# Optimization experiments

Measured on AMD Instinct MI355X. Metric: run time of the kernel, lower is better.

The kernel has to match this reference:

```python
import jax, jax.numpy as jnp
import numpy as np

HEADS = 8

def setup_inputs() -> dict:
    key = jax.random.key(0)
    ks = jax.random.split(key, 6)
    d = 256
    x = jax.random.normal(ks[0], (1, 8, 96, 96, d), dtype=jnp.float32)
    w_qkv = jax.random.normal(ks[1], (3 * d, d), dtype=jnp.float32) * (d ** -0.5)
    w_out = jax.random.normal(ks[2], (d, d), dtype=jnp.float32) * (d ** -0.5)
    b_out = jax.random.normal(ks[3], (d,), dtype=jnp.float32) * 0.01
    w_lin = jax.random.normal(ks[4], (d, d), dtype=jnp.float32) * (d ** -0.5)
    b_lin = jax.random.normal(ks[5], (d,), dtype=jnp.float32) * 0.01
    return {"x": x, "w_qkv": w_qkv, "w_out": w_out, "b_out": b_out,
            "w_lin": w_lin, "b_lin": b_lin}


def reference(x, w_qkv, w_out, b_out, w_lin, b_lin):
    b, t, h, w, d = x.shape
    dh = d // HEADS
    scale = dh ** -0.5
    n = h * w
    # fold time into batch; per-frame spatial tokens: [bf, n, d]
    xf = x.reshape(b * t, n, d)
    # 1x1 conv to_qkv (no bias) == matmul
    qkv = jnp.einsum('bnd,ed->bne', xf, w_qkv)          # [bf, n, 3d]
    q, k, v = jnp.split(qkv, 3, axis=-1)
    def to_heads(z):  # 'b (h c) xy' head-major split -> [bf, H, dh, n]
        return z.reshape(b * t, n, HEADS, dh).transpose(0, 2, 3, 1)
    q, k, v = map(to_heads, (q, k, v))
    q = jax.nn.softmax(q, axis=-2) * scale              # softmax over channel dim
    k = jax.nn.softmax(k, axis=-1)                      # softmax over spatial dim
    ctx = jnp.einsum('bhdn,bhen->bhde', k, v)           # [bf, H, dh, dh]
    out = jnp.einsum('bhde,bhdn->bhen', ctx, q)         # [bf, H, dh, n]
    out = out.transpose(0, 3, 1, 2).reshape(b * t, n, HEADS * dh)  # head-major merge
    out = out @ w_out.T + b_out                          # to_out 1x1 conv
    out = out.reshape(b, t, h, w, d)
    out = out @ w_lin.T + b_lin                          # fresh nn.Linear(d, d)
    return out + x                                       # residual skip
```

## Files before the change

kernel.cpp:

```cpp
#include <hip/hip_runtime.h>

using u16 = unsigned short;
typedef __attribute__((ext_vector_type(8))) short short8;
typedef __attribute__((ext_vector_type(4))) float f32x4;

__device__ __forceinline__ float b2f(u16 u){ union{unsigned u; float f;} c; c.u = ((unsigned)u) << 16; return c.f; }
__device__ __forceinline__ u16 f2b(float f){
  union{float f; unsigned u;} c; c.f = f;
  unsigned r = 0x7fffu + ((c.u >> 16) & 1u);
  return (u16)((c.u + r) >> 16);
}

#define GLOAD_LDS16(g, l) __builtin_amdgcn_global_load_lds( \
  (const __attribute__((address_space(1))) unsigned int*)(g), \
  (__attribute__((address_space(3))) unsigned int*)(l), 16, 0, 0)

__global__ void k_cvt(const float4* __restrict__ in, ushort4* __restrict__ out, int n4){
  int i = blockIdx.x * 256 + threadIdx.x;
  if (i < n4){
    float4 v = in[i];
    ushort4 o; o.x = f2b(v.x); o.y = f2b(v.y); o.z = f2b(v.z); o.w = f2b(v.w);
    out[i] = o;
  }
}

__global__ __launch_bounds__(256) void k_cvtw(const float* __restrict__ w, u16* __restrict__ out){
  int r = blockIdx.x, c = threadIdx.x;
  int src;
  if (r < 256) src = r;
  else { int g = r - 256, p4 = g >> 7, o = g & 127;
         src = (o < 64) ? 256 + p4*64 + o : 512 + p4*64 + (o - 64); }
  out[r*256 + c] = f2b(w[src*256 + c]);
}

__global__ __launch_bounds__(256) void k_prepw(const float* __restrict__ w_lin, const float* __restrict__ w_out,
    const float* __restrict__ b_out, const float* __restrict__ b_lin,
    float* __restrict__ wcf, float* __restrict__ bc){
  int l = blockIdx.x, i = threadIdx.x;
  float s = 0.f;
  for (int j = 0; j < 256; ++j) s += w_lin[l*256 + j] * w_out[j*256 + i];
  wcf[l*256 + i] = s;
  __shared__ float red[256];
  red[i] = w_lin[l*256 + i] * b_out[i];
  __syncthreads();
  for (int off = 128; off > 0; off >>= 1){ if (i < off) red[i] += red[i + off]; __syncthreads(); }
  if (i == 0) bc[l] = red[0] + b_lin[l];
}

__global__ __launch_bounds__(256, 3) void k_gemm_qkv(const u16* __restrict__ A, const u16* __restrict__ B,
    u16* __restrict__ qs, float* __restrict__ ctxu, float* __restrict__ zu, int M){
  constexpr int K = 256, NT = 8;
  __shared__ __align__(16) u16 pool[24576];
  u16* As = pool;
  u16* Bs = pool + 12288;
  const int t = threadIdx.x;
  const int wave = t >> 6, lane = t & 63;
  const int bi = blockIdx.x;
  const int xk = bi & 7, bj = bi >> 3;
  const int bm = (xk + 8*(bj/6)) * 128;
  const int bn = bj % 6;
  const int srow = wave*32 + (lane>>2);
  const int skel = (((lane&3) ^ ((lane>>3)&3)) << 3);
  const u16* ag = A + (size_t)(bm + srow)*K + skel;
  const u16* bg = B + (size_t)(bn*128 + srow)*K + skel;
  const size_t rstep = (size_t)16*K;
  const int wr = (wave>>1)*64, wc4 = (wave&1)*64;
  const int fr = lane & 15;
  const int fkc = lane >> 4;
  const int koff = ((fkc ^ ((fr>>1)&3)) << 3);
  f32x4 acc[4][4] = {};
  #pragma unroll
  for (int pre = 0; pre < 2; ++pre){
    u16* asl = As + pre*4096 + wave*1024; u16* bsl = Bs + pre*4096 + wave*1024;
    const int k0 = pre*32;
    GLOAD_LDS16(ag + k0,         asl);
    GLOAD_LDS16(ag + rstep + k0, asl + 512);
    GLOAD_LDS16(bg + k0,         bsl);
    GLOAD_LDS16(bg + rstep + k0, bsl + 512);
  }
  #pragma unroll
  for (int it = 0; it < NT; ++it){
    const int cur = it % 3;
    if (it == NT-1) { asm volatile("s_waitcnt vmcnt(0)" ::: "memory"); }
    else            { asm volatile("s_waitcnt vmcnt(4)" ::: "memory"); }
    __builtin_amdgcn_s_barrier();
    __builtin_amdgcn_sched_barrier(0);
    short8 av[4], bv[4];
    #pragma unroll
    for (int m = 0; m < 4; ++m)
      av[m] = *(const short8*)&As[cur*4096 + (wr + m*16 + fr)*32 + koff];
    #pragma unroll
    for (int n = 0; n < 4; ++n)
      bv[n] = *(const short8*)&Bs[cur*4096 + (wc4 + n*16 + fr)*32 + koff];
    if (it + 2 < NT){
      const int nb = (it+2) % 3;
      u16* asl = As + nb*4096 + wave*1024; u16* bsl = Bs + nb*4096 + wave*1024;
      const int k0 = (it+2)*32;
      GLOAD_LDS16(ag + k0,         asl);
      GLOAD_LDS16(ag + rstep + k0, asl + 512);
      GLOAD_LDS16(bg + k0,         bsl);
      GLOAD_LDS16(bg + rstep + k0, bsl + 512);
    }
    __builtin_amdgcn_s_setprio(1);
    #pragma unroll
    for (int m = 0; m < 4; ++m)
      #pragma unroll
      for (int n = 0; n < 4; ++n)
        acc[m][n] = __builtin_amdgcn_mfma_f32_16x16x32_bf16(av[m], bv[n], acc[m][n], 0, 0, 0);
    __builtin_amdgcn_s_setprio(0);
  }
  __syncthreads();
  const int lr0 = wr + (lane>>4)*4;
  if (bn < 2){
    u16* cmat = pool;
    #pragma unroll
    for (int m = 0; m < 4; ++m)
      #pragma unroll
      for (int n = 0; n < 4; ++n)
        #pragma unroll
        for (int r = 0; r < 4; ++r)
          cmat[(lr0 + m*16 + r)*136 + wc4 + n*16 + fr] = f2b(acc[m][n][r]);
    __syncthreads();
    const int row = t >> 1, co = (t & 1) * 64;
    #pragma unroll
    for (int hh = 0; hh < 2; ++hh){
      float f[32];
      #pragma unroll
      for (int c4 = 0; c4 < 4; ++c4){
        short8 w = *(const short8*)&cmat[row*136 + co + hh*32 + c4*8];
        #pragma unroll
        for (int k2 = 0; k2 < 8; ++k2) f[c4*8+k2] = b2f((u16)w[k2]);
      }
      float sum = 0.f;
      #pragma unroll
      for (int i2 = 0; i2 < 32; ++i2){ float e = __expf(f[i2]); f[i2] = e; sum += e; }
      float sc = 0.17677669529663689f / sum;
      #pragma unroll
      for (int c4 = 0; c4 < 4; ++c4){
        short8 o;
        #pragma unroll
        for (int k2 = 0; k2 < 8; ++k2) o[k2] = (short)f2b(f[c4*8+k2] * sc);
        *(short8*)&qs[(size_t)(bm+row)*256 + bn*128 + co + hh*32 + c4*8] = o;
      }
    }
  } else {
    u16* ekT = pool;
    u16* vT  = pool + 64*136;
    const bool isK = (wc4 == 0);
    #pragma unroll
    for (int m = 0; m < 4; ++m)
      #pragma unroll
      for (int n = 0; n < 4; ++n)
        #pragma unroll
        for (int r = 0; r < 4; ++r){
          int row = lr0 + m*16 + r;
          int csub = n*16 + fr;
          if (isK) ekT[csub*136 + row] = f2b(__expf(acc[m][n][r]));
          else     vT [csub*136 + row] = f2b(acc[m][n][r]);
        }
    __syncthreads();
    const int hl = wave >> 1, ti = wave & 1;
    const int head = (bn - 2)*2 + hl;
    short8 ones;
    #pragma unroll
    for (int j = 0; j < 8; ++j) ones[j] = (short)0x3F80;
    f32x4 acc2[2] = {}; f32x4 zacc = {};
    #pragma unroll
    for (int kc = 0; kc < 4; ++kc){
      const int ko2 = kc*32 + fkc*8;
      short8 av2 = *(const short8*)&ekT[(hl*32 + ti*16 + fr)*136 + ko2];
      short8 bv0 = *(const short8*)&vT [(hl*32 +         fr)*136 + ko2];
      short8 bv1 = *(const short8*)&vT [(hl*32 + 16 +    fr)*136 + ko2];
      acc2[0] = __builtin_amdgcn_mfma_f32_16x16x32_bf16(av2, bv0, acc2[0], 0, 0, 0);
      acc2[1] = __builtin_amdgcn_mfma_f32_16x16x32_bf16(av2, bv1, acc2[1], 0, 0, 0);
      zacc    = __builtin_amdgcn_mfma_f32_16x16x32_bf16(av2, ones, zacc, 0, 0, 0);
    }
    const int frame = bm / 9216;
    float* cb = ctxu + ((size_t)frame*8 + head)*1024;
    const int drow = ti*16 + (lane>>4)*4;
    #pragma unroll
    for (int tj = 0; tj < 2; ++tj)
      #pragma unroll
      for (int rr = 0; rr < 4; ++rr)
        atomicAdd(&cb[(drow + rr)*32 + tj*16 + fr], acc2[tj][rr]);
    if (fr == 0){
      float* zb = zu + ((size_t)frame*8 + head)*32;
      #pragma unroll
      for (int rr = 0; rr < 4; ++rr)
        atomicAdd(&zb[drow + rr], zacc[rr]);
    }
  }
}

__global__ __launch_bounds__(256, 3) void k_gemm_out(const u16* __restrict__ A, const u16* __restrict__ B,
    float* __restrict__ Cf, const float* __restrict__ bias, const u16* __restrict__ residb,
    int M, int NB, int frame_rows){
  constexpr int K = 256, N = 256, NT = 8;
  __shared__ __align__(16) u16 pool[24576];
  u16* As = pool;
  u16* Bs = pool + 12288;
  const int t = threadIdx.x;
  const int wave = t >> 6, lane = t & 63;
  const int bi = blockIdx.x;
  const int xk = bi & 7, bj = bi >> 3;
  const int bm = (xk + 8*(bj/NB)) * 128, bn = (bj%NB) * 128;
  if (frame_rows > 0) B += (size_t)(bm / frame_rows) * N * K;
  const int srow = wave*32 + (lane>>2);
  const int skel = (((lane&3) ^ ((lane>>3)&3)) << 3);
  const u16* ag = A + (size_t)(bm + srow)*K + skel;
  const u16* bg = B + (size_t)(bn + srow)*K + skel;
  const size_t rstep = (size_t)16*K;
  const int wr = (wave>>1)*64, wc4 = (wave&1)*64;
  const int fr = lane & 15;
  const int fkc = lane >> 4;
  const int koff = ((fkc ^ ((fr>>1)&3)) << 3);
  f32x4 acc[4][4] = {};
  #pragma unroll
  for (int pre = 0; pre < 2; ++pre){
    u16* asl = As + pre*4096 + wave*1024; u16* bsl = Bs + pre*4096 + wave*1024;
    const int k0 = pre*32;
    GLOAD_LDS16(ag + k0,         asl);
    GLOAD_LDS16(ag + rstep + k0, asl + 512);
    GLOAD_LDS16(bg + k0,         bsl);
    GLOAD_LDS16(bg + rstep + k0, bsl + 512);
  }
  #pragma unroll
  for (int it = 0; it < NT; ++it){
    const int cur = it % 3;
    if (it == NT-1) { asm volatile("s_waitcnt vmcnt(0)" ::: "memory"); }
    else            { asm volatile("s_waitcnt vmcnt(4)" ::: "memory"); }
    __builtin_amdgcn_s_barrier();
    __builtin_amdgcn_sched_barrier(0);
    short8 av[4], bv[4];
    #pragma unroll
    for (int m = 0; m < 4; ++m)
      av[m] = *(const short8*)&As[cur*4096 + (wr + m*16 + fr)*32 + koff];
    #pragma unroll
    for (int n = 0; n < 4; ++n)
      bv[n] = *(const short8*)&Bs[cur*4096 + (wc4 + n*16 + fr)*32 + koff];
    if (it + 2 < NT){
      const int nb = (it+2) % 3;
      u16* asl = As + nb*4096 + wave*1024; u16* bsl = Bs + nb*4096 + wave*1024;
      const int k0 = (it+2)*32;
      GLOAD_LDS16(ag + k0,         asl);
      GLOAD_LDS16(ag + rstep + k0, asl + 512);
      GLOAD_LDS16(bg + k0,         bsl);
      GLOAD_LDS16(bg + rstep + k0, bsl + 512);
    }
    __builtin_amdgcn_s_setprio(1);
    #pragma unroll
    for (int m = 0; m < 4; ++m)
      #pragma unroll
      for (int n = 0; n < 4; ++n)
        acc[m][n] = __builtin_amdgcn_mfma_f32_16x16x32_bf16(av[m], bv[n], acc[m][n], 0, 0, 0);
    __builtin_amdgcn_s_setprio(0);
  }
  __syncthreads();
  float* cmatf = (float*)pool;
  const int lr0 = (lane>>4)*4;
  float biasr[32];
  {
    const int c0 = bn + (t&3)*32;
    #pragma unroll
    for (int c4 = 0; c4 < 8; ++c4)
      *(float4*)&biasr[c4*4] = *(const float4*)&bias[c0 + c4*4];
  }
  #pragma unroll
  for (int half = 0; half < 2; ++half){
    if ((wr >> 6) == half){
      #pragma unroll
      for (int m = 0; m < 4; ++m)
        #pragma unroll
        for (int n = 0; n < 4; ++n)
          #pragma unroll
          for (int r = 0; r < 4; ++r)
            cmatf[(lr0 + m*16 + r)*132 + wc4 + n*16 + fr] = acc[m][n][r];
    }
    __syncthreads();
    {
      const int row = t >> 2, seg = (t & 3) * 32;
      const int gr = bm + half*64 + row;
      const size_t gbase = (size_t)gr*256 + bn + seg;
      float v[32];
      #pragma unroll
      for (int c4 = 0; c4 < 8; ++c4)
        *(float4*)&v[c4*4] = *(const float4*)&cmatf[row*132 + seg + c4*4];
      #pragma unroll
      for (int c4 = 0; c4 < 4; ++c4){
        short8 rr = *(const short8*)&residb[gbase + c4*8];
        #pragma unroll
        for (int k2 = 0; k2 < 8; ++k2)
          v[c4*8+k2] += biasr[c4*8+k2] + b2f((u16)rr[k2]);
      }
      #pragma unroll
      for (int c4 = 0; c4 < 8; ++c4)
        *(float4*)&Cf[gbase + c4*4] = *(float4*)&v[c4*4];
    }
    __syncthreads();
  }
}

__global__ __launch_bounds__(256) void k_weff(const float* __restrict__ ctxu, const float* __restrict__ zu,
    const float* __restrict__ wcf, u16* __restrict__ weff){
  int l = blockIdx.x, frel = blockIdx.y, t = threadIdx.x;
  int h = t >> 5, dd = t & 31;
  const float* cr = ctxu + (size_t)frel*8192 + h*1024 + dd*32;
  const float* wr = wcf + (size_t)l*256 + h*32;
  float s = 0.f;
  #pragma unroll
  for (int e = 0; e < 32; ++e) s += cr[e] * wr[e];
  float iz = 1.0f / zu[frel*256 + t];
  weff[((size_t)frel*256 + l)*256 + t] = f2b(s * iz);
}

extern "C" void kernel_launch(void* const* d_in, const int* in_sizes, int n_in,
                              void* d_out, int out_size, void* d_ws, size_t ws_size,
                              hipStream_t stream){
  const float* x     = (const float*)d_in[0];
  const float* w_qkv = (const float*)d_in[1];
  const float* w_out = (const float*)d_in[2];
  const float* b_out = (const float*)d_in[3];
  const float* w_lin = (const float*)d_in[4];
  const float* b_lin = (const float*)d_in[5];
  float* out = (float*)d_out;

  char* p = (char*)d_ws;
  u16*   wqb   = (u16*)p;   p += (size_t)768*256*2;
  float* wcf   = (float*)p; p += (size_t)256*256*4;
  float* bc    = (float*)p; p += 256*4;
  float* ctxu  = (float*)p; p += (size_t)8*8192*4;
  float* zu    = (float*)p; p += (size_t)8*256*4;
  u16*   weffb = (u16*)p;   p += (size_t)8*256*256*2;
  size_t fixed = (size_t)(p - (char*)d_ws);
  size_t per_frame = (size_t)2 * 9216*256*2;
  int chunk = (ws_size >= fixed + 8*per_frame) ? 8 : 1;
  u16* xb  = (u16*)p;
  u16* qsb = xb  + (size_t)chunk*9216*256;

  hipMemsetAsync(ctxu, 0, (size_t)8*8192*4 + (size_t)8*256*4, stream);

  hipLaunchKernelGGL(k_cvtw, dim3(768), dim3(256), 0, stream, w_qkv, wqb);
  hipLaunchKernelGGL(k_prepw, dim3(256), dim3(256), 0, stream, w_lin, w_out, b_out, b_lin, wcf, bc);

  for (int f0 = 0; f0 < 8; f0 += chunk){
    const float* xc = x  + (size_t)f0*9216*256;
    float*       oc = out + (size_t)f0*9216*256;
    const int M = chunk * 9216;
    const int n4 = M * 256 / 4;
    hipLaunchKernelGGL(k_cvt, dim3((n4 + 255)/256), dim3(256), 0, stream, (const float4*)xc, (ushort4*)xb, n4);
    hipLaunchKernelGGL(k_gemm_qkv, dim3((M/128)*6), dim3(256), 0, stream,
                       xb, wqb, qsb, ctxu + (size_t)f0*8192, zu + (size_t)f0*256, M);
    hipLaunchKernelGGL(k_weff, dim3(256, chunk), dim3(256), 0, stream,
                       ctxu + (size_t)f0*8192, zu + (size_t)f0*256, wcf, weffb + (size_t)f0*256*256);
    hipLaunchKernelGGL(k_gemm_out, dim3((M/128)*2), dim3(256), 0, stream,
                       qsb, weffb + (size_t)f0*256*256, oc, bc, xb,
                       M, 2, (chunk == 8) ? 9216 : 0);
  }
}
```

Before: 146.6 us.

## Spread ctx atomics over 8 slots, pack LDS stores, merge prep kernels

Atomic accumulation of the per-frame context and normaliser now goes to one of 8 replicated slots chosen by row tile, which reduces contention on each address. k_weff sums the slots before the projection. The K/V transpose stores into LDS are packed as 4 bf16 values in a uint2 instead of scalar u16 writes. The two weight-prep kernels are merged into one launch. The cost is a larger memset and slot reduction reads in k_weff.

```diff
diff --git a/kernel.cpp b/kernel.cpp
--- a/kernel.cpp
+++ b/kernel.cpp
@@ -24,27 +24,28 @@
   }
 }
 
-__global__ __launch_bounds__(256) void k_cvtw(const float* __restrict__ w, u16* __restrict__ out){
-  int r = blockIdx.x, c = threadIdx.x;
-  int src;
-  if (r < 256) src = r;
-  else { int g = r - 256, p4 = g >> 7, o = g & 127;
-         src = (o < 64) ? 256 + p4*64 + o : 512 + p4*64 + (o - 64); }
-  out[r*256 + c] = f2b(w[src*256 + c]);
-}
-
-__global__ __launch_bounds__(256) void k_prepw(const float* __restrict__ w_lin, const float* __restrict__ w_out,
+__global__ __launch_bounds__(256) void k_prep(const float* __restrict__ w,
+    const float* __restrict__ w_lin, const float* __restrict__ w_out,
     const float* __restrict__ b_out, const float* __restrict__ b_lin,
-    float* __restrict__ wcf, float* __restrict__ bc){
-  int l = blockIdx.x, i = threadIdx.x;
-  float s = 0.f;
-  for (int j = 0; j < 256; ++j) s += w_lin[l*256 + j] * w_out[j*256 + i];
-  wcf[l*256 + i] = s;
-  __shared__ float red[256];
-  red[i] = w_lin[l*256 + i] * b_out[i];
-  __syncthreads();
-  for (int off = 128; off > 0; off >>= 1){ if (i < off) red[i] += red[i + off]; __syncthreads(); }
-  if (i == 0) bc[l] = red[0] + b_lin[l];
+    u16* __restrict__ wq, float* __restrict__ wcf, float* __restrict__ bc){
+  int r = blockIdx.x, i = threadIdx.x;
+  if (r < 768){
+    int src;
+    if (r < 256) src = r;
+    else { int g = r - 256, p4 = g >> 7, o = g & 127;
+           src = (o < 64) ? 256 + p4*64 + o : 512 + p4*64 + (o - 64); }
+    wq[r*256 + i] = f2b(w[src*256 + i]);
+  } else {
+    int l = r - 768;
+    float s = 0.f;
+    for (int j = 0; j < 256; ++j) s += w_lin[l*256 + j] * w_out[j*256 + i];
+    wcf[l*256 + i] = s;
+    __shared__ float red[256];
+    red[i] = w_lin[l*256 + i] * b_out[i];
+    __syncthreads();
+    for (int off = 128; off > 0; off >>= 1){ if (i < off) red[i] += red[i + off]; __syncthreads(); }
+    if (i == 0) bc[l] = red[0] + b_lin[l];
+  }
 }
 
 __global__ __launch_bounds__(256, 3) void k_gemm_qkv(const u16* __restrict__ A, const u16* __restrict__ B,
@@ -147,17 +148,23 @@
     u16* ekT = pool;
     u16* vT  = pool + 64*136;
     const bool isK = (wc4 == 0);
-    #pragma unroll
-    for (int m = 0; m < 4; ++m)
-      #pragma unroll
-      for (int n = 0; n < 4; ++n)
-        #pragma unroll
-        for (int r = 0; r < 4; ++r){
-          int row = lr0 + m*16 + r;
-          int csub = n*16 + fr;
-          if (isK) ekT[csub*136 + row] = f2b(__expf(acc[m][n][r]));
-          else     vT [csub*136 + row] = f2b(acc[m][n][r]);
+    u16* dst = isK ? ekT : vT;
+    #pragma unroll
+    for (int m = 0; m < 4; ++m)
+      #pragma unroll
+      for (int n = 0; n < 4; ++n){
+        const int row = lr0 + m*16;
+        const int csub = n*16 + fr;
+        uint2 pk;
+        if (isK){
+          pk.x = (unsigned)f2b(__expf(acc[m][n][0])) | ((unsigned)f2b(__expf(acc[m][n][1])) << 16);
+          pk.y = (unsigned)f2b(__expf(acc[m][n][2])) | ((unsigned)f2b(__expf(acc[m][n][3])) << 16);
+        } else {
+          pk.x = (unsigned)f2b(acc[m][n][0]) | ((unsigned)f2b(acc[m][n][1]) << 16);
+          pk.y = (unsigned)f2b(acc[m][n][2]) | ((unsigned)f2b(acc[m][n][3]) << 16);
         }
+        *(uint2*)&dst[csub*136 + row] = pk;
+      }
     __syncthreads();
     const int hl = wave >> 1, ti = wave & 1;
     const int head = (bn - 2)*2 + hl;
@@ -176,7 +183,8 @@
       zacc    = __builtin_amdgcn_mfma_f32_16x16x32_bf16(av2, ones, zacc, 0, 0, 0);
     }
     const int frame = bm / 9216;
-    float* cb = ctxu + ((size_t)frame*8 + head)*1024;
+    const int slot = ((bm % 9216) >> 7) & 7;
+    float* cb = ctxu + (((size_t)frame*8 + slot)*8 + head)*1024;
     const int drow = ti*16 + (lane>>4)*4;
     #pragma unroll
     for (int tj = 0; tj < 2; ++tj)
@@ -184,7 +192,7 @@
       for (int rr = 0; rr < 4; ++rr)
         atomicAdd(&cb[(drow + rr)*32 + tj*16 + fr], acc2[tj][rr]);
     if (fr == 0){
-      float* zb = zu + ((size_t)frame*8 + head)*32;
+      float* zb = zu + (((size_t)frame*8 + slot)*8 + head)*32;
       #pragma unroll
       for (int rr = 0; rr < 4; ++rr)
         atomicAdd(&zb[drow + rr], zacc[rr]);
@@ -304,13 +312,23 @@
     const float* __restrict__ wcf, u16* __restrict__ weff){
   int l = blockIdx.x, frel = blockIdx.y, t = threadIdx.x;
   int h = t >> 5, dd = t & 31;
-  const float* cr = ctxu + (size_t)frel*8192 + h*1024 + dd*32;
+  float c[32];
+  #pragma unroll
+  for (int e = 0; e < 32; ++e) c[e] = 0.f;
+  #pragma unroll
+  for (int sl = 0; sl < 8; ++sl){
+    const float* cr = ctxu + (((size_t)frel*8 + sl)*8 + h)*1024 + dd*32;
+    #pragma unroll
+    for (int e = 0; e < 32; ++e) c[e] += cr[e];
+  }
+  float z = 0.f;
+  #pragma unroll
+  for (int sl = 0; sl < 8; ++sl) z += zu[(((size_t)frel*8 + sl)*8 + h)*32 + dd];
   const float* wr = wcf + (size_t)l*256 + h*32;
   float s = 0.f;
   #pragma unroll
-  for (int e = 0; e < 32; ++e) s += cr[e] * wr[e];
-  float iz = 1.0f / zu[frel*256 + t];
-  weff[((size_t)frel*256 + l)*256 + t] = f2b(s * iz);
+  for (int e = 0; e < 32; ++e) s += c[e] * wr[e];
+  weff[((size_t)frel*256 + l)*256 + t] = f2b(s / z);
 }
 
 extern "C" void kernel_launch(void* const* d_in, const int* in_sizes, int n_in,
@@ -328,8 +346,8 @@
   u16*   wqb   = (u16*)p;   p += (size_t)768*256*2;
   float* wcf   = (float*)p; p += (size_t)256*256*4;
   float* bc    = (float*)p; p += 256*4;
-  float* ctxu  = (float*)p; p += (size_t)8*8192*4;
-  float* zu    = (float*)p; p += (size_t)8*256*4;
+  float* ctxu  = (float*)p; p += (size_t)8*8*8192*4;
+  float* zu    = (float*)p; p += (size_t)8*8*256*4;
   u16*   weffb = (u16*)p;   p += (size_t)8*256*256*2;
   size_t fixed = (size_t)(p - (char*)d_ws);
   size_t per_frame = (size_t)2 * 9216*256*2;
@@ -337,10 +355,10 @@
   u16* xb  = (u16*)p;
   u16* qsb = xb  + (size_t)chunk*9216*256;
 
-  hipMemsetAsync(ctxu, 0, (size_t)8*8192*4 + (size_t)8*256*4, stream);
-
-  hipLaunchKernelGGL(k_cvtw, dim3(768), dim3(256), 0, stream, w_qkv, wqb);
-  hipLaunchKernelGGL(k_prepw, dim3(256), dim3(256), 0, stream, w_lin, w_out, b_out, b_lin, wcf, bc);
+  hipMemsetAsync(ctxu, 0, (size_t)8*8*8192*4 + (size_t)8*8*256*4, stream);
+
+  hipLaunchKernelGGL(k_prep, dim3(1024), dim3(256), 0, stream,
+                     w_qkv, w_lin, w_out, b_out, b_lin, wqb, wcf, bc);
 
   for (int f0 = 0; f0 < 8; f0 += chunk){
     const float* xc = x  + (size_t)f0*9216*256;
@@ -349,9 +367,9 @@
     const int n4 = M * 256 / 4;
     hipLaunchKernelGGL(k_cvt, dim3((n4 + 255)/256), dim3(256), 0, stream, (const float4*)xc, (ushort4*)xb, n4);
     hipLaunchKernelGGL(k_gemm_qkv, dim3((M/128)*6), dim3(256), 0, stream,
-                       xb, wqb, qsb, ctxu + (size_t)f0*8192, zu + (size_t)f0*256, M);
+                       xb, wqb, qsb, ctxu + (size_t)f0*8*8192, zu + (size_t)f0*8*256, M);
     hipLaunchKernelGGL(k_weff, dim3(256, chunk), dim3(256), 0, stream,
-                       ctxu + (size_t)f0*8192, zu + (size_t)f0*256, wcf, weffb + (size_t)f0*256*256);
+                       ctxu + (size_t)f0*8*8192, zu + (size_t)f0*8*256, wcf, weffb + (size_t)f0*256*256);
     hipLaunchKernelGGL(k_gemm_out, dim3((M/128)*2), dim3(256), 0, stream,
                        qsb, weffb + (size_t)f0*256*256, oc, bc, xb,
                        M, 2, (chunk == 8) ? 9216 : 0);
```

Result: slower. 219.2 us (+49.5%).
